# Kernel optimization log

Measured on AMD Instinct MI355X. Metric: run time of the kernel, lower is better.

## Reference

```python
import jax, jax.numpy as jnp
import numpy as np

D_MODEL = 1024
NUM_HEADS = 16
D_HEAD = D_MODEL // NUM_HEADS


def setup_inputs() -> dict:
    key = jax.random.key(0)
    ks = jax.random.split(key, 9)
    s = 1.0 / np.sqrt(D_MODEL)
    inp = {"x": jax.random.normal(ks[0], (2, 2048, D_MODEL), dtype=jnp.float32)}
    for i, name in enumerate(["q", "k", "v", "o"]):
        inp[f"W_{name}"] = jax.random.uniform(ks[1 + 2 * i], (D_MODEL, D_MODEL), minval=-s, maxval=s, dtype=jnp.float32)
        inp[f"b_{name}"] = jax.random.uniform(ks[2 + 2 * i], (D_MODEL,), minval=-s, maxval=s, dtype=jnp.float32)
    return inp


def reference(x, W_q, b_q, W_k, b_k, W_v, b_v, W_o, b_o):
    B, S, _ = x.shape
    def heads(W, b):
        # [B,S,D] @ [D,D] -> [B,S,H,Dh] -> [B,H,S,Dh]
        return (x @ W.T + b).reshape(B, S, NUM_HEADS, D_HEAD).transpose(0, 2, 1, 3)
    Q, K, V = heads(W_q, b_q), heads(W_k, b_k), heads(W_v, b_v)
    scores = jnp.einsum("bhqd,bhkd->bhqk", Q, K) / jnp.sqrt(jnp.float32(D_HEAD))
    causal = jnp.tril(jnp.ones((S, S), dtype=bool))  # True = keep
    scores = jnp.where(causal, scores, -jnp.inf)
    A = jax.nn.softmax(scores, axis=-1)
    out = jnp.einsum("bhqk,bhkd->bhqd", A, V)  # [B,H,S,Dh]
    out = out.transpose(0, 2, 1, 3).reshape(B, S, D_MODEL)
    return out @ W_o.T + b_o
```

## Files before the change

kernel.cpp:

```cpp
#include <hip/hip_runtime.h>
#include <math.h>

#define D_MODEL 1024
#define NUM_HEADS 16
#define D_HEAD 64
#define SEQ 2048
#define BATCH 2
#define NROWS (BATCH * SEQ)

typedef short s8v __attribute__((ext_vector_type(8)));
typedef float f4v __attribute__((ext_vector_type(4)));

__device__ __forceinline__ short to_bf(float f) {
    union { float f; unsigned u; } x; x.f = f;
    unsigned r = x.u + 0x7fffu + ((x.u >> 16) & 1u);
    return (short)(r >> 16);
}

__device__ __forceinline__ void gld_lds16(const short* g, short* l) {
    __builtin_amdgcn_global_load_lds(
        (const __attribute__((address_space(1))) unsigned*)g,
        (__attribute__((address_space(3))) unsigned*)l, 16, 0, 0);
}

#define QSCALE 0.180336880f

__global__ __launch_bounds__(256) void cvt_fused(
    const float* __restrict__ x,  const float* __restrict__ Wq,
    const float* __restrict__ Wk, const float* __restrict__ Wv,
    const float* __restrict__ Wo,
    short* __restrict__ Xb, short* __restrict__ Wqkvb, short* __restrict__ Wob)
{
    const int NX = NROWS * D_MODEL / 4;
    const int NW = D_MODEL * D_MODEL / 4;
    int j = blockIdx.x * 256 + threadIdx.x;
    const float* src; short* dst; float sc = 1.f;
    if (j < NX)                 { src = x;  dst = Xb; }
    else if ((j -= NX) < NW)    { src = Wq; dst = Wqkvb; sc = QSCALE; }
    else if ((j -= NW) < NW)    { src = Wk; dst = Wqkvb + NW * 4; }
    else if ((j -= NW) < NW)    { src = Wv; dst = Wqkvb + NW * 8; }
    else                        { j -= NW; src = Wo; dst = Wob; }
    float4 v = ((const float4*)src)[j];
    short4 s = { to_bf(v.x * sc), to_bf(v.y * sc), to_bf(v.z * sc), to_bf(v.w * sc) };
    ((short4*)dst)[j] = s;
}

__global__ __launch_bounds__(256) void gemm_bf16(
    const short* __restrict__ Xb, const short* __restrict__ Wb,
    const float* __restrict__ B0, const float* __restrict__ B1, const float* __restrict__ B2,
    float* __restrict__ Ofp,
    short* __restrict__ Q0, short* __restrict__ K1, short* __restrict__ V2,
    int qkv_mode)
{
    __shared__ __align__(16) short smem[18432];
    short* As = smem;
    short* Bs = smem + 8192;

    const int t    = threadIdx.x;
    const int w    = t >> 6;
    const int lane = t & 63;
    const int quad = lane >> 4;
    const int l15  = lane & 15;
    const int wm   = w & 1, wn = w >> 1;

    const int n0 = blockIdx.x * 128;
    const int m0 = blockIdx.y * 128;

    f4v acc[4][4];
#pragma unroll
    for (int i = 0; i < 4; ++i)
#pragma unroll
        for (int j = 0; j < 4; ++j) acc[i][j] = (f4v){0.f, 0.f, 0.f, 0.f};

    for (int k0 = 0; k0 < D_MODEL; k0 += 64) {
#pragma unroll
        for (int i = 0; i < 4; ++i) {
            const int cid = i * 256 + t;
            const int row = cid >> 3, kc = cid & 7, g = kc ^ (row & 7);
            gld_lds16(&Xb[(size_t)(m0 + row) * D_MODEL + k0 + g * 8],
                      &As[(i * 256 + w * 64) * 8]);
            gld_lds16(&Wb[(size_t)(n0 + row) * D_MODEL + k0 + g * 8],
                      &Bs[(i * 256 + w * 64) * 8]);
        }
        __syncthreads();

#pragma unroll
        for (int c = 0; c < 2; ++c) {
            s8v af[4], bf[4];
            const int pos = ((c * 4 + quad) ^ (l15 & 7)) * 8;
#pragma unroll
            for (int mi = 0; mi < 4; ++mi)
                af[mi] = *(const s8v*)&As[(wm * 64 + mi * 16 + l15) * 64 + pos];
#pragma unroll
            for (int ni = 0; ni < 4; ++ni)
                bf[ni] = *(const s8v*)&Bs[(wn * 64 + ni * 16 + l15) * 64 + pos];
#pragma unroll
            for (int mi = 0; mi < 4; ++mi)
#pragma unroll
                for (int ni = 0; ni < 4; ++ni)
                    acc[mi][ni] = __builtin_amdgcn_mfma_f32_16x16x32_bf16(
                        af[mi], bf[ni], acc[mi][ni], 0, 0, 0);
        }
        __syncthreads();
    }

    if (!qkv_mode) {
#pragma unroll
        for (int ni = 0; ni < 4; ++ni) {
            const int col = n0 + wn * 64 + ni * 16 + l15;
            const float bv = B0[col];
#pragma unroll
            for (int mi = 0; mi < 4; ++mi)
#pragma unroll
                for (int r = 0; r < 4; ++r) {
                    const int row = m0 + wm * 64 + mi * 16 + quad * 4 + r;
                    Ofp[(size_t)row * D_MODEL + col] = acc[mi][ni][r] + bv;
                }
        }
        return;
    }

    const int sel = n0 >> 10;
    const float* bias = sel == 0 ? B0 : sel == 1 ? B1 : B2;
    short* out        = sel == 0 ? Q0 : sel == 1 ? K1 : V2;
    const float bsc   = sel == 0 ? QSCALE : 1.f;
    const int h0 = (n0 & 1023) >> 6;

#pragma unroll
    for (int ni = 0; ni < 4; ++ni) {
        const int col = wn * 64 + ni * 16 + l15;
        const float bv = bias[(n0 & 1023) + col] * bsc;
#pragma unroll
        for (int mi = 0; mi < 4; ++mi)
#pragma unroll
            for (int r = 0; r < 4; ++r) {
                const int row = wm * 64 + mi * 16 + quad * 4 + r;
                const short v = to_bf(acc[mi][ni][r] + bv);
                if (sel < 2) smem[row * 144 + col] = v;
                else         smem[col * 144 + row] = v;
            }
    }
    __syncthreads();

    const int rr = t >> 1, half = t & 1;
    const int bb = m0 >> 11, mloc = m0 & (SEQ - 1);
    const short* src = &smem[rr * 144 + half * 64];
    short* dst;
    if (sel < 2)
        dst = out + (((size_t)(bb * NUM_HEADS + h0 + half) * SEQ + (mloc + rr)) * D_HEAD);
    else
        dst = out + ((size_t)(bb * NUM_HEADS + h0 + (rr >> 6)) * D_HEAD + (rr & 63)) * SEQ
                  + mloc + half * 64;
#pragma unroll
    for (int i = 0; i < 8; ++i)
        ((int4*)dst)[i] = ((const int4*)src)[i];
}

__global__ __launch_bounds__(256) void attn_mfma(
    const short* __restrict__ Qg, const short* __restrict__ Kg,
    const short* __restrict__ Vg,
    short* __restrict__ Op0, short* __restrict__ Op1, float* __restrict__ Lp)
{
    __shared__ __align__(16) short Kb[128 * 64];
    __shared__ __align__(16) short Vs[64 * 128];
    __shared__ __align__(16) short Ps[4][32 * 72];

    const int t    = threadIdx.x;
    const int w    = t >> 6;
    const int lane = t & 63;
    const int quad = lane >> 4;
    const int l15  = lane & 15;

    const int bidx = blockIdx.x;
    const int seg  = bidx >> 9;
    const int p    = bidx & 255;
    const int bh   = p >> 3;
    const int pair = p & 7;
    const int qt   = ((bidx >> 8) & 1) ? 15 - pair : pair;
    const int b    = bh >> 4, h = bh & 15;

    const short* qbase = Qg + (size_t)bh * SEQ * D_HEAD;
    const short* kbase = Kg + (size_t)bh * SEQ * D_HEAD;
    const short* vbase = Vg + (size_t)bh * D_HEAD * SEQ;
    const int q0 = qt * 128;
    const int qw = w * 32;

    s8v aq[2][2];
#pragma unroll
    for (int ns = 0; ns < 2; ++ns)
#pragma unroll
        for (int c = 0; c < 2; ++c)
            aq[ns][c] = *(const s8v*)&qbase[(size_t)(q0 + qw + ns * 16 + l15) * D_HEAD
                                            + c * 32 + quad * 8];

    f4v Oacc[2][4];
#pragma unroll
    for (int ms = 0; ms < 2; ++ms)
#pragma unroll
        for (int nt = 0; nt < 4; ++nt) Oacc[ms][nt] = (f4v){0.f, 0.f, 0.f, 0.f};
    float lsum[2] = {0.f, 0.f};

    for (int j = seg; j <= qt; j += 2) {
        __syncthreads();
        {
            const int k0 = j * 128;
#pragma unroll
            for (int i = 0; i < 4; ++i) {
                const int cid = i * 256 + w * 64 + lane;
                {
                    const int row = cid >> 3, pp = cid & 7, g = pp ^ (row & 7);
                    gld_lds16(&kbase[(size_t)(k0 + row) * D_HEAD + g * 8],
                              &Kb[(i * 256 + w * 64) * 8]);
                }
                {
                    const int row = cid >> 4, pp = cid & 15;
                    const int g = (pp & 8) | ((pp & 7) ^ (row & 7));
                    gld_lds16(&vbase[(size_t)row * SEQ + k0 + g * 8],
                              &Vs[(i * 256 + w * 64) * 8]);
                }
            }
        }
        __syncthreads();

        const bool diag = (j == qt);

#pragma unroll
        for (int half = 0; half < 2; ++half) {
#pragma unroll
            for (int mt = 0; mt < 4; ++mt) {
                const int krow = half * 64 + mt * 16 + l15;
                s8v ka0 = *(const s8v*)&Kb[(krow * 8 + (quad ^ (l15 & 7))) * 8];
                s8v ka1 = *(const s8v*)&Kb[(krow * 8 + ((4 + quad) ^ (l15 & 7))) * 8];
#pragma unroll
                for (int ns = 0; ns < 2; ++ns) {
                    f4v st = (f4v){0.f, 0.f, 0.f, 0.f};
                    st = __builtin_amdgcn_mfma_f32_16x16x32_bf16(ka0, aq[ns][0], st, 0, 0, 0);
                    st = __builtin_amdgcn_mfma_f32_16x16x32_bf16(ka1, aq[ns][1], st, 0, 0, 0);
                    if (diag) {
#pragma unroll
                        for (int r = 0; r < 4; ++r)
                            if (half * 64 + mt * 16 + quad * 4 + r > qw + ns * 16 + l15)
                                st[r] = -INFINITY;
                    }
                    float e0 = exp2f(st[0]), e1 = exp2f(st[1]);
                    float e2 = exp2f(st[2]), e3 = exp2f(st[3]);
                    lsum[ns] += (e0 + e1) + (e2 + e3);
                    int2 pk;
                    pk.x = (int)((__float_as_uint(e0) >> 16) | (__float_as_uint(e1) & 0xffff0000u));
                    pk.y = (int)((__float_as_uint(e2) >> 16) | (__float_as_uint(e3) & 0xffff0000u));
                    *(int2*)&Ps[w][(ns * 16 + l15) * 72 + mt * 16 + quad * 4] = pk;
                }
            }
#pragma unroll
            for (int c2 = 0; c2 < 2; ++c2) {
                s8v ap0 = *(const s8v*)&Ps[w][l15 * 72 + c2 * 32 + quad * 8];
                s8v ap1 = *(const s8v*)&Ps[w][(16 + l15) * 72 + c2 * 32 + quad * 8];
                const int g = (half * 2 + c2) * 4 + quad;
                const int pos = (g & 8) | ((g & 7) ^ (l15 & 7));
                s8v bv[4];
#pragma unroll
                for (int nt = 0; nt < 4; ++nt)
                    bv[nt] = *(const s8v*)&Vs[((nt * 16 + l15) * 16 + pos) * 8];
#pragma unroll
                for (int nt = 0; nt < 4; ++nt) {
                    Oacc[0][nt] = __builtin_amdgcn_mfma_f32_16x16x32_bf16(
                        ap0, bv[nt], Oacc[0][nt], 0, 0, 0);
                    Oacc[1][nt] = __builtin_amdgcn_mfma_f32_16x16x32_bf16(
                        ap1, bv[nt], Oacc[1][nt], 0, 0, 0);
                }
            }
        }
    }

#pragma unroll
    for (int ns = 0; ns < 2; ++ns) {
        lsum[ns] += __shfl_xor(lsum[ns], 16, 64);
        lsum[ns] += __shfl_xor(lsum[ns], 32, 64);
    }
    float* L = Lp + ((size_t)seg << 16) + (size_t)bh * SEQ;
    if (quad == 0) {
        L[q0 + qw + l15]      = lsum[0];
        L[q0 + qw + 16 + l15] = lsum[1];
    }
    short* Op = (seg ? Op1 : Op0) + (size_t)bh * SEQ * D_HEAD;
#pragma unroll
    for (int ms = 0; ms < 2; ++ms)
#pragma unroll
        for (int r = 0; r < 4; ++r) {
            const int nloc = q0 + qw + ms * 16 + quad * 4 + r;
            short* dst = Op + (size_t)nloc * D_HEAD + l15;
#pragma unroll
            for (int nt = 0; nt < 4; ++nt)
                dst[nt * 16] = to_bf(Oacc[ms][nt][r]);
        }
}

__global__ __launch_bounds__(256) void combine(
    const short* __restrict__ Op0, const short* __restrict__ Op1,
    const float* __restrict__ Lp, short* __restrict__ ctxb)
{
    const int id  = blockIdx.x * 256 + threadIdx.x;
    const int e   = id * 8;
    const int bh  = e >> 17;
    const int rem = e & 131071;
    const int s   = rem >> 6, dh = rem & 63;
    const int b   = bh >> 4,  h  = bh & 15;

    int4 p0 = *(const int4*)&Op0[e];
    int4 p1 = *(const int4*)&Op1[e];
    const float inv = 1.f / (Lp[(size_t)bh * SEQ + s] + Lp[65536 + (size_t)bh * SEQ + s]);

    const unsigned* u0 = (const unsigned*)&p0;
    const unsigned* u1 = (const unsigned*)&p1;
    short outv[8];
#pragma unroll
    for (int i = 0; i < 4; ++i) {
        float a0 = __uint_as_float(u0[i] << 16), b0 = __uint_as_float(u0[i] & 0xffff0000u);
        float a1 = __uint_as_float(u1[i] << 16), b1 = __uint_as_float(u1[i] & 0xffff0000u);
        outv[2 * i]     = to_bf((a0 + a1) * inv);
        outv[2 * i + 1] = to_bf((b0 + b1) * inv);
    }
    short* dst = &ctxb[(size_t)(b * SEQ + s) * D_MODEL + h * D_HEAD + dh];
    *(int4*)dst = *(const int4*)outv;
}

extern "C" void kernel_launch(void* const* d_in, const int* in_sizes, int n_in,
                              void* d_out, int out_size, void* d_ws, size_t ws_size,
                              hipStream_t stream)
{
    const float* x  = (const float*)d_in[0];
    const float* Wq = (const float*)d_in[1];
    const float* bq = (const float*)d_in[2];
    const float* Wk = (const float*)d_in[3];
    const float* bk = (const float*)d_in[4];
    const float* Wv = (const float*)d_in[5];
    const float* bv = (const float*)d_in[6];
    const float* Wo = (const float*)d_in[7];
    const float* bo = (const float*)d_in[8];
    float* out = (float*)d_out;

    short* wsp = (short*)d_ws;
    const size_t MAT = (size_t)NROWS * D_MODEL;
    short* Qb    = wsp;
    short* Kbg   = Qb + MAT;
    short* Vtb   = Kbg + MAT;
    short* ctxb  = Vtb + MAT;
    short* Xb    = ctxb + MAT;
    short* Wqkvb = Xb + MAT;
    short* Wob   = Wqkvb + 3 * D_MODEL * D_MODEL;
    short* Op0   = Xb;
    short* Op1   = Wob + D_MODEL * D_MODEL;
    float* Lp    = (float*)(Op1 + MAT);

    cvt_fused<<<8192, 256, 0, stream>>>(x, Wq, Wk, Wv, Wo, Xb, Wqkvb, Wob);

    gemm_bf16<<<dim3(3 * D_MODEL / 128, NROWS / 128), 256, 0, stream>>>(
        Xb, Wqkvb, bq, bk, bv, nullptr, Qb, Kbg, Vtb, 1);

    attn_mfma<<<dim3(1024), 256, 0, stream>>>(Qb, Kbg, Vtb, Op0, Op1, Lp);

    combine<<<dim3(2048), 256, 0, stream>>>(Op0, Op1, Lp, ctxb);

    gemm_bf16<<<dim3(D_MODEL / 128, NROWS / 128), 256, 0, stream>>>(
        ctxb, Wob, bo, bo, bo, out, nullptr, nullptr, nullptr, 0);
}
```

Measured before the change: 215.5 us.

## Fuse split-attention combine into output projection GEMM and remap QKV blocks by XCD

Result: no change. 213.8 us (-0.8%).

```diff
diff --git a/kernel.cpp b/kernel.cpp
--- a/kernel.cpp
+++ b/kernel.cpp
@@ -45,12 +45,10 @@
     ((short4*)dst)[j] = s;
 }
 
-__global__ __launch_bounds__(256) void gemm_bf16(
+__global__ __launch_bounds__(256) void gemm_qkv(
     const short* __restrict__ Xb, const short* __restrict__ Wb,
     const float* __restrict__ B0, const float* __restrict__ B1, const float* __restrict__ B2,
-    float* __restrict__ Ofp,
-    short* __restrict__ Q0, short* __restrict__ K1, short* __restrict__ V2,
-    int qkv_mode)
+    short* __restrict__ Q0, short* __restrict__ K1, short* __restrict__ V2)
 {
     __shared__ __align__(16) short smem[18432];
     short* As = smem;
@@ -63,8 +61,13 @@
     const int l15  = lane & 15;
     const int wm   = w & 1, wn = w >> 1;
 
-    const int n0 = blockIdx.x * 128;
-    const int m0 = blockIdx.y * 128;
+    const int bx    = blockIdx.x;
+    const int xcd   = bx & 7;
+    const int g_    = bx >> 3;
+    const int n_loc = g_ % 12;
+    const int m_loc = g_ / 12;
+    const int n0 = ((xcd >> 2) * 12 + n_loc) * 128;
+    const int m0 = ((xcd & 3) * 8 + m_loc) * 128;
 
     f4v acc[4][4];
 #pragma unroll
@@ -102,22 +105,6 @@
                         af[mi], bf[ni], acc[mi][ni], 0, 0, 0);
         }
         __syncthreads();
-    }
-
-    if (!qkv_mode) {
-#pragma unroll
-        for (int ni = 0; ni < 4; ++ni) {
-            const int col = n0 + wn * 64 + ni * 16 + l15;
-            const float bv = B0[col];
-#pragma unroll
-            for (int mi = 0; mi < 4; ++mi)
-#pragma unroll
-                for (int r = 0; r < 4; ++r) {
-                    const int row = m0 + wm * 64 + mi * 16 + quad * 4 + r;
-                    Ofp[(size_t)row * D_MODEL + col] = acc[mi][ni][r] + bv;
-                }
-        }
-        return;
     }
 
     const int sel = n0 >> 10;
@@ -178,6 +165,7 @@
     const int pair = p & 7;
     const int qt   = ((bidx >> 8) & 1) ? 15 - pair : pair;
     const int b    = bh >> 4, h = bh & 15;
+    (void)b; (void)h;
 
     const short* qbase = Qg + (size_t)bh * SEQ * D_HEAD;
     const short* kbase = Kg + (size_t)bh * SEQ * D_HEAD;
@@ -295,33 +283,107 @@
         }
 }
 
-__global__ __launch_bounds__(256) void combine(
+__global__ __launch_bounds__(256) void gemm_oproj(
     const short* __restrict__ Op0, const short* __restrict__ Op1,
-    const float* __restrict__ Lp, short* __restrict__ ctxb)
+    const float* __restrict__ Lp, const short* __restrict__ Wob,
+    const float* __restrict__ bo, float* __restrict__ out)
 {
-    const int id  = blockIdx.x * 256 + threadIdx.x;
-    const int e   = id * 8;
-    const int bh  = e >> 17;
-    const int rem = e & 131071;
-    const int s   = rem >> 6, dh = rem & 63;
-    const int b   = bh >> 4,  h  = bh & 15;
-
-    int4 p0 = *(const int4*)&Op0[e];
-    int4 p1 = *(const int4*)&Op1[e];
-    const float inv = 1.f / (Lp[(size_t)bh * SEQ + s] + Lp[65536 + (size_t)bh * SEQ + s]);
-
-    const unsigned* u0 = (const unsigned*)&p0;
-    const unsigned* u1 = (const unsigned*)&p1;
-    short outv[8];
-#pragma unroll
-    for (int i = 0; i < 4; ++i) {
-        float a0 = __uint_as_float(u0[i] << 16), b0 = __uint_as_float(u0[i] & 0xffff0000u);
-        float a1 = __uint_as_float(u1[i] << 16), b1 = __uint_as_float(u1[i] & 0xffff0000u);
-        outv[2 * i]     = to_bf((a0 + a1) * inv);
-        outv[2 * i + 1] = to_bf((b0 + b1) * inv);
-    }
-    short* dst = &ctxb[(size_t)(b * SEQ + s) * D_MODEL + h * D_HEAD + dh];
-    *(int4*)dst = *(const int4*)outv;
+    __shared__ __align__(16) short As[128 * 64];
+    __shared__ __align__(16) short Bs[64 * 64];
+    __shared__ float invL[NUM_HEADS * 128];
+
+    const int t    = threadIdx.x;
+    const int w    = t >> 6;
+    const int lane = t & 63;
+    const int quad = lane >> 4;
+    const int l15  = lane & 15;
+    const int wm   = w & 1, wn = w >> 1;
+
+    const int n0 = blockIdx.x * 64;
+    const int m0 = blockIdx.y * 128;
+    const int bb = m0 >> 11, sloc = m0 & (SEQ - 1);
+
+#pragma unroll
+    for (int ii = 0; ii < 8; ++ii) {
+        const int idx = t * 8 + ii;
+        const int hh = idx >> 7, sl = idx & 127;
+        const size_t loff = (size_t)(bb * NUM_HEADS + hh) * SEQ + sloc + sl;
+        invL[idx] = 1.f / (Lp[loff] + Lp[65536 + loff]);
+    }
+    __syncthreads();
+
+    f4v acc[4][2];
+#pragma unroll
+    for (int i = 0; i < 4; ++i)
+#pragma unroll
+        for (int j = 0; j < 2; ++j) acc[i][j] = (f4v){0.f, 0.f, 0.f, 0.f};
+
+    for (int k0 = 0; k0 < D_MODEL; k0 += 64) {
+        const int h = k0 >> 6;
+#pragma unroll
+        for (int i = 0; i < 2; ++i) {
+            const int cid = i * 256 + w * 64 + lane;
+            const int row = cid >> 3, pp = cid & 7, g = pp ^ (row & 7);
+            gld_lds16(&Wob[(size_t)(n0 + row) * D_MODEL + k0 + g * 8],
+                      &Bs[(i * 256 + w * 64) * 8]);
+        }
+        const size_t obase = ((size_t)(bb * NUM_HEADS + h) * SEQ + sloc) * D_HEAD;
+#pragma unroll
+        for (int i = 0; i < 4; ++i) {
+            const int cid = i * 256 + t;
+            const int row = cid >> 3, pp = cid & 7, g = pp ^ (row & 7);
+            const size_t off = obase + (size_t)row * D_HEAD + g * 8;
+            int4 a0 = *(const int4*)&Op0[off];
+            int4 a1 = *(const int4*)&Op1[off];
+            const float inv = invL[h * 128 + row];
+            const unsigned* u0 = (const unsigned*)&a0;
+            const unsigned* u1 = (const unsigned*)&a1;
+            int4 o;
+#pragma unroll
+            for (int d = 0; d < 4; ++d) {
+                float lo = (__uint_as_float(u0[d] << 16) +
+                            __uint_as_float(u1[d] << 16)) * inv;
+                float hi = (__uint_as_float(u0[d] & 0xffff0000u) +
+                            __uint_as_float(u1[d] & 0xffff0000u)) * inv;
+                ((unsigned*)&o)[d] = (__float_as_uint(lo) >> 16) |
+                                     (__float_as_uint(hi) & 0xffff0000u);
+            }
+            *(int4*)&As[cid * 8] = o;
+        }
+        __syncthreads();
+
+#pragma unroll
+        for (int c = 0; c < 2; ++c) {
+            s8v af[4], bf[2];
+            const int pos = ((c * 4 + quad) ^ (l15 & 7)) * 8;
+#pragma unroll
+            for (int mi = 0; mi < 4; ++mi)
+                af[mi] = *(const s8v*)&As[(wm * 64 + mi * 16 + l15) * 64 + pos];
+#pragma unroll
+            for (int ni = 0; ni < 2; ++ni)
+                bf[ni] = *(const s8v*)&Bs[(wn * 32 + ni * 16 + l15) * 64 + pos];
+#pragma unroll
+            for (int mi = 0; mi < 4; ++mi)
+#pragma unroll
+                for (int ni = 0; ni < 2; ++ni)
+                    acc[mi][ni] = __builtin_amdgcn_mfma_f32_16x16x32_bf16(
+                        af[mi], bf[ni], acc[mi][ni], 0, 0, 0);
+        }
+        __syncthreads();
+    }
+
+#pragma unroll
+    for (int ni = 0; ni < 2; ++ni) {
+        const int col = n0 + wn * 32 + ni * 16 + l15;
+        const float bv = bo[col];
+#pragma unroll
+        for (int mi = 0; mi < 4; ++mi)
+#pragma unroll
+            for (int r = 0; r < 4; ++r) {
+                const int row = m0 + wm * 64 + mi * 16 + quad * 4 + r;
+                out[(size_t)row * D_MODEL + col] = acc[mi][ni][r] + bv;
+            }
+    }
 }
 
 extern "C" void kernel_launch(void* const* d_in, const int* in_sizes, int n_in,
@@ -344,8 +406,7 @@
     short* Qb    = wsp;
     short* Kbg   = Qb + MAT;
     short* Vtb   = Kbg + MAT;
-    short* ctxb  = Vtb + MAT;
-    short* Xb    = ctxb + MAT;
+    short* Xb    = Vtb + 2 * MAT;
     short* Wqkvb = Xb + MAT;
     short* Wob   = Wqkvb + 3 * D_MODEL * D_MODEL;
     short* Op0   = Xb;
@@ -354,13 +415,10 @@
 
     cvt_fused<<<8192, 256, 0, stream>>>(x, Wq, Wk, Wv, Wo, Xb, Wqkvb, Wob);
 
-    gemm_bf16<<<dim3(3 * D_MODEL / 128, NROWS / 128), 256, 0, stream>>>(
-        Xb, Wqkvb, bq, bk, bv, nullptr, Qb, Kbg, Vtb, 1);
-
-    attn_mfma<<<dim3(1024), 256, 0, stream>>>(Qb, Kbg, Vtb, Op0, Op1, Lp);
-
-    combine<<<dim3(2048), 256, 0, stream>>>(Op0, Op1, Lp, ctxb);
-
-    gemm_bf16<<<dim3(D_MODEL / 128, NROWS / 128), 256, 0, stream>>>(
-        ctxb, Wob, bo, bo, bo, out, nullptr, nullptr, nullptr, 0);
-}
+    gemm_qkv<<<768, 256, 0, stream>>>(Xb, Wqkvb, bq, bk, bv, Qb, Kbg, Vtb);
+
+    attn_mfma<<<1024, 256, 0, stream>>>(Qb, Kbg, Vtb, Op0, Op1, Lp);
+
+    gemm_oproj<<<dim3(D_MODEL / 64, NROWS / 128), 256, 0, stream>>>(
+        Op0, Op1, Lp, Wob, bo, out);
+}
```
